# Optimization experiments

Measured on AMD Instinct MI355X. Metric: run time of the kernel, lower is better.

The kernel has to match this reference:

```python
import jax, jax.numpy as jnp
import numpy as np

D_MODEL = 1024
NUM_HEADS = 16
D_K = D_MODEL // NUM_HEADS
ROPE_THETA = 10000.0


def setup_inputs() -> dict:
    key = jax.random.key(0)
    kx, kq, kk, kv, ko = jax.random.split(key, 5)
    B, S = 4, 2048
    std = (2.0 / (D_MODEL + D_MODEL)) ** 0.5
    def w(k):
        return jax.random.truncated_normal(k, -3.0, 3.0, (D_MODEL, D_MODEL), jnp.float32) * std
    return {
        "x": jax.random.normal(kx, (B, S, D_MODEL), jnp.float32),
        "Wq": w(kq), "Wk": w(kk), "Wv": w(kv), "Wo": w(ko),
    }


def _apply_rope(t):
    # t: [B, H, S, d_k]
    S, dk = t.shape[-2], t.shape[-1]
    inv_freq = 1.0 / (ROPE_THETA ** (jnp.arange(0, dk, 2) / dk))  # [dk/2]
    angles = jnp.outer(jnp.arange(S), inv_freq)                    # [S, dk/2]
    cos = jnp.repeat(jnp.cos(angles), 2, axis=-1).astype(t.dtype)  # [S, dk]
    sin = jnp.repeat(jnp.sin(angles), 2, axis=-1).astype(t.dtype)
    t_even = t[..., 0::2]
    t_odd = t[..., 1::2]
    t_rot = jnp.stack([-t_odd, t_even], axis=-1).reshape(t.shape)
    return t * cos + t_rot * sin


def reference(x, Wq, Wk, Wv, Wo):
    B, S, D = x.shape
    H, dk = NUM_HEADS, D_K
    q = jnp.einsum("bsi,io->bso", x, Wq).reshape(B, S, H, dk).swapaxes(1, 2)
    k = jnp.einsum("bsi,io->bso", x, Wk).reshape(B, S, H, dk).swapaxes(1, 2)
    v = jnp.einsum("bsi,io->bso", x, Wv).reshape(B, S, H, dk).swapaxes(1, 2)
    q = _apply_rope(q)
    k = _apply_rope(k)
    scores = jnp.einsum("bhqd,bhkd->bhqk", q, k) / (dk ** 0.5)  # [B,H,S,S]
    causal = jnp.tril(jnp.ones((S, S), dtype=bool))
    scores = jnp.where(causal, scores, -jnp.inf)
    attn = jax.nn.softmax(scores, axis=-1)
    out = jnp.einsum("bhqk,bhkd->bhqd", attn, v)  # [B,H,S,dk]
    out = out.swapaxes(1, 2).reshape(B, S, D)
    return jnp.einsum("bsi,io->bso", out, Wo)
```

## Files before the change

kernel.cpp:

```cpp
#include <hip/hip_runtime.h>
#include <hip/hip_bf16.h>

#define SEQ   2048
#define NB    4
#define NH    16
#define DK    64
#define DM    1024
#define MROWS (NB * SEQ)

typedef __bf16 bf16_t;
typedef __bf16 bf16x8 __attribute__((ext_vector_type(8)));
typedef __bf16 bf16x4 __attribute__((ext_vector_type(4)));
typedef float  f32x4  __attribute__((ext_vector_type(4)));

#define MFMA16(a, b, c) __builtin_amdgcn_mfma_f32_16x16x32_bf16((a), (b), (c), 0, 0, 0)

__device__ __forceinline__ void gl2lds16(const bf16_t* g, bf16_t* l) {
    __builtin_amdgcn_global_load_lds(
        (const __attribute__((address_space(1))) unsigned int*)g,
        (__attribute__((address_space(3))) unsigned int*)l, 16, 0, 0);
}

#define SBAR()   asm volatile("s_barrier" ::: "memory")
#define VMC(N)   asm volatile("s_waitcnt vmcnt(" #N ")" ::: "memory")

__global__ __launch_bounds__(256) void cvt_kernel(
    const float* __restrict__ in, bf16_t* __restrict__ out, int n)
{
    int i = (blockIdx.x * 256 + threadIdx.x) * 4;
    if (i + 3 < n) {
        const float4 v = *(const float4*)(in + i);
        bf16x4 o;
        o[0] = (bf16_t)v.x; o[1] = (bf16_t)v.y;
        o[2] = (bf16_t)v.z; o[3] = (bf16_t)v.w;
        *(bf16x4*)(out + i) = o;
    }
}

__global__ __launch_bounds__(256) void wtr_kernel(
    const float* __restrict__ W, bf16_t* __restrict__ Wt)
{
    __shared__ float T[32][33];
    const int tk0 = (blockIdx.x >> 5) << 5;
    const int tn0 = (blockIdx.x & 31) << 5;
    const int r = threadIdx.x >> 5, c = threadIdx.x & 31;
#pragma unroll
    for (int i = 0; i < 4; ++i)
        T[r + i * 8][c] = W[(size_t)(tk0 + r + i * 8) * DM + tn0 + c];
    __syncthreads();
#pragma unroll
    for (int i = 0; i < 4; ++i)
        Wt[(size_t)(tn0 + r + i * 8) * DM + tk0 + c] = (bf16_t)T[c][r + i * 8];
}

__global__ void rope_table_kernel(float2* __restrict__ tab) {
    int idx = blockIdx.x * 256 + threadIdx.x;
    if (idx >= SEQ * 32) return;
    int s = idx >> 5, i = idx & 31;
    float freq = powf(10000.0f, -(float)i / 32.0f);
    float a = (float)s * freq;
    tab[idx] = make_float2(cosf(a), sinf(a));
}

template<bool TR>
__device__ __forceinline__ void kloop(
    const bf16_t* __restrict__ Xp, const bf16_t* __restrict__ Wp,
    bf16_t* L, int tid, f32x4 (&acc)[8][4])
{
    const int lane = tid & 63;
    const int wave = tid >> 6;
    const int wm   = wave >> 2;
    const int wn   = wave & 3;
    const int lrow = lane & 15;
    const int lcol = (lane >> 4) << 3;

    bf16_t* const AR = L;
    bf16_t* const BR = L + 32768;

    const bf16_t* pA0 = Xp + (size_t)(wave * 16 + lrow) * DM + lcol;
    const bf16_t* pA1 = pA0 + (size_t)128 * DM;
    const bf16_t* pB0 = Wp + (size_t)(wave * 16 + lrow) * DM + lcol;
    const bf16_t* pB1 = pB0 + (size_t)128 * DM;

    bf16_t* const adst = AR + wave * 1024;
    bf16_t* const bdst = BR + wave * 1024;

    const bf16_t* const Ard = AR + wm * 8192;
    const bf16_t* const Brd = BR + wn * 4096;

    bf16x8 a0[2][2], a1[2][2], bc[4][2], bn[4][2];

#define RD_A(BUF, Q, D)                                                       \
    D[0][0] = *(const bf16x8*)(Ard + (BUF) + (2*(Q)+0)*1024 + lane*8);        \
    D[0][1] = *(const bf16x8*)(Ard + (BUF) + (2*(Q)+0)*1024 + 512 + lane*8);  \
    D[1][0] = *(const bf16x8*)(Ard + (BUF) + (2*(Q)+1)*1024 + lane*8);        \
    D[1][1] = *(const bf16x8*)(Ard + (BUF) + (2*(Q)+1)*1024 + 512 + lane*8);

#define RD_B(BUF, NF, D)                                                      \
    D[NF][0] = *(const bf16x8*)(Brd + (BUF) + (NF)*1024 + lane*8);            \
    D[NF][1] = *(const bf16x8*)(Brd + (BUF) + (NF)*1024 + 512 + lane*8);

#define ST_A(BUF, H, C)                                                       \
    gl2lds16(((H) ? pA1 : pA0) + (C),      adst + (BUF) + (H)*8192);          \
    gl2lds16(((H) ? pA1 : pA0) + (C) + 32, adst + (BUF) + (H)*8192 + 512);

#define ST_B(BUF, H, C)                                                       \
    gl2lds16(((H) ? pB1 : pB0) + (C),      bdst + (BUF) + (H)*8192);          \
    gl2lds16(((H) ? pB1 : pB0) + (C) + 32, bdst + (BUF) + (H)*8192 + 512);

#define QMMA(Q, A, B)                                                         \
    __builtin_amdgcn_s_setprio(1);                                            \
    _Pragma("unroll")                                                         \
    for (int nf = 0; nf < 4; ++nf) {                                          \
        if (TR) {                                                             \
            acc[2*(Q)][nf]   = MFMA16(B[nf][0], A[0][0], acc[2*(Q)][nf]);     \
            acc[2*(Q)][nf]   = MFMA16(B[nf][1], A[0][1], acc[2*(Q)][nf]);     \
            acc[2*(Q)+1][nf] = MFMA16(B[nf][0], A[1][0], acc[2*(Q)+1][nf]);   \
            acc[2*(Q)+1][nf] = MFMA16(B[nf][1], A[1][1], acc[2*(Q)+1][nf]);   \
        } else {                                                              \
            acc[2*(Q)][nf]   = MFMA16(A[0][0], B[nf][0], acc[2*(Q)][nf]);     \
            acc[2*(Q)][nf]   = MFMA16(A[0][1], B[nf][1], acc[2*(Q)][nf]);     \
            acc[2*(Q)+1][nf] = MFMA16(A[1][0], B[nf][0], acc[2*(Q)+1][nf]);   \
            acc[2*(Q)+1][nf] = MFMA16(A[1][1], B[nf][1], acc[2*(Q)+1][nf]);   \
        }                                                                     \
    }                                                                         \
    __builtin_amdgcn_s_setprio(0);

#define ITER(LST)                                                             \
                                                              \
    VMC(4); SBAR();                                                           \
    RD_A(0, 1, a1) RD_B(16384, 0, bn)                                         \
    if (!(LST)) { ST_B(0, 0, 128) }                                           \
    QMMA(0, a0, bc)                                                           \
                                                              \
    SBAR();                                                                   \
    RD_A(0, 2, a0) RD_B(16384, 1, bn)                                         \
    if (!(LST)) { ST_B(0, 1, 128) }                                           \
    QMMA(1, a1, bc)                                                           \
                                                              \
    SBAR();                                                                   \
    RD_A(0, 3, a1) RD_B(16384, 2, bn)                                         \
    QMMA(2, a0, bc)                                                           \
                                                              \
    if (LST) { VMC(0); } else { VMC(4); }                                     \
    SBAR();                                                                   \
    RD_A(16384, 0, a0) RD_B(16384, 3, bn)                                     \
    if (!(LST)) { ST_A(0, 0, 128) }                                           \
    QMMA(3, a1, bc)                                                           \
                                                            \
    if (!(LST)) { VMC(2); }                                                   \
    SBAR();                                                                   \
    RD_A(16384, 1, a1) RD_B(0, 0, bc)                                         \
    if (!(LST)) { ST_A(0, 1, 128) }                                           \
    QMMA(0, a0, bn)                                                           \
                                                            \
    SBAR();                                                                   \
    RD_A(16384, 2, a0) RD_B(0, 1, bc)                                         \
    if (!(LST)) { ST_B(16384, 0, 192) }                                       \
    QMMA(1, a1, bn)                                                           \
                                                            \
    SBAR();                                                                   \
    RD_A(16384, 3, a1) RD_B(0, 2, bc)                                         \
    if (!(LST)) { ST_B(16384, 1, 192) }                                       \
    QMMA(2, a0, bn)                                                           \
                                                            \
    if (!(LST)) { VMC(4); }                                                   \
    SBAR();                                                                   \
    RD_A(0, 0, a0) RD_B(0, 3, bc)                                             \
    if (!(LST)) { ST_A(16384, 0, 192) ST_A(16384, 1, 192) }                   \
    QMMA(3, a1, bn)

    ST_A(0, 0, 0) ST_A(0, 1, 0)
    ST_B(0, 0, 0) ST_B(0, 1, 0)
    ST_B(16384, 0, 64) ST_B(16384, 1, 64)
    ST_A(16384, 0, 64) ST_A(16384, 1, 64)
    VMC(8);
    SBAR();
    RD_A(0, 0, a0)
    RD_B(0, 0, bc) RD_B(0, 1, bc) RD_B(0, 2, bc) RD_B(0, 3, bc)

    for (int it = 0; it < 7; ++it) {
        ITER(0)
        pA0 += 128; pA1 += 128; pB0 += 128; pB1 += 128;
    }
    ITER(1)

#undef ITER
#undef QMMA
#undef ST_B
#undef ST_A
#undef RD_B
#undef RD_A
}

__global__ __launch_bounds__(512, 2) void gemm_qkv_kernel(
    const bf16_t* __restrict__ X, const bf16_t* __restrict__ Wt,
    bf16_t* __restrict__ Qt, bf16_t* __restrict__ Kt, bf16_t* __restrict__ Vtr,
    const float2* __restrict__ rope)
{
    __shared__ __align__(16) bf16_t L[65536];

    const int tid = threadIdx.x;
    const int xcd = blockIdx.x & 7;
    const int idx = blockIdx.x >> 3;
    const int mt  = xcd * 4 + (idx & 3);
    const int nt  = idx >> 2;
    const int m0 = mt << 8, n0 = nt << 8;
    const bool tr = (n0 >= 2 * DM);

    f32x4 acc[8][4] = {};
    if (tr) kloop<true >(X + (size_t)m0 * DM, Wt + (size_t)n0 * DM, L, tid, acc);
    else    kloop<false>(X + (size_t)m0 * DM, Wt + (size_t)n0 * DM, L, tid, acc);

    const int lane = tid & 63;
    const int wave = tid >> 6;
    const int wm   = wave >> 2, wn = wave & 3;
    const int l    = lane & 15;
    const int quad = lane >> 4;

#pragma unroll
    for (int mf = 0; mf < 8; ++mf)
#pragma unroll
        for (int nf = 0; nf < 4; ++nf)
#pragma unroll
            for (int r = 0; r < 4; ++r) {
                float v = acc[mf][nf][r];
                if (tr) {
                    const int n = n0 + wn * 64 + nf * 16 + quad * 4 + r;
                    const int m = m0 + wm * 128 + mf * 16 + l;
                    const int bi = m >> 11, s = m & (SEQ - 1);
                    const int col = n & (DM - 1);
                    const int h = col >> 6, d = col & (DK - 1);
                    Vtr[(((size_t)(bi * NH + h)) * DK + d) * SEQ + s] = (bf16_t)v;
                } else {
                    const int m  = m0 + wm * 128 + mf * 16 + quad * 4 + r;
                    const int nn = n0 + wn * 64 + nf * 16 + l;
                    const int bi = m >> 11, s = m & (SEQ - 1);
                    const int col = nn & (DM - 1);
                    const int h = col >> 6, d = col & (DK - 1);
                    float pv = __shfl_xor(v, 1);
                    float2 cs = rope[s * 32 + (d >> 1)];
                    float res = (d & 1) ? (v * cs.x + pv * cs.y)
                                        : (v * cs.x - pv * cs.y);
                    bf16_t* dst = (nn < DM) ? Qt : Kt;
                    if (nn < DM) res *= 0.125f;
                    dst[(((size_t)(bi * NH + h)) * SEQ + s) * DK + d] = (bf16_t)res;
                }
            }
}

__global__ __launch_bounds__(512, 2) void gemm_out_kernel(
    const bf16_t* __restrict__ X, const bf16_t* __restrict__ Wt,
    float* __restrict__ out)
{
    __shared__ __align__(16) bf16_t L[65536];

    const int tid = threadIdx.x;
    const int xcd = blockIdx.x & 7;
    const int idx = blockIdx.x >> 3;
    const int mt  = xcd * 4 + (idx & 3);
    const int nt  = idx >> 2;
    const int m0 = mt << 8, n0 = nt << 8;

    f32x4 acc[8][4] = {};
    kloop<false>(X + (size_t)m0 * DM, Wt + (size_t)n0 * DM, L, tid, acc);

    const int lane = tid & 63;
    const int wave = tid >> 6;
    const int wm   = wave >> 2, wn = wave & 3;
    const int l    = lane & 15;
    const int quad = lane >> 4;

#pragma unroll
    for (int mf = 0; mf < 8; ++mf)
#pragma unroll
        for (int nf = 0; nf < 4; ++nf)
#pragma unroll
            for (int r = 0; r < 4; ++r) {
                const int m  = m0 + wm * 128 + mf * 16 + quad * 4 + r;
                const int nn = n0 + wn * 64 + nf * 16 + l;
                out[(size_t)m * DM + nn] = acc[mf][nf][r];
            }
}

#define KLD 72

__global__ __launch_bounds__(256) void attn_kernel(
    const bf16_t* __restrict__ Q, const bf16_t* __restrict__ K,
    const bf16_t* __restrict__ Vt, bf16_t* __restrict__ O)
{
    __shared__ __align__(16) bf16_t Kl[64 * KLD];
    __shared__ __align__(16) bf16_t Vl[64 * KLD];
    __shared__ __align__(16) bf16_t Pl[4][32 * KLD];

    const int bh   = blockIdx.x;
    const int qx   = blockIdx.y;
    const int tid  = threadIdx.x;
    const int wave = tid >> 6;
    const int lane = tid & 63;
    const int l    = lane & 15;
    const int quad = lane >> 4;
    const int srow = tid >> 3;
    const int sch  = (tid & 7) << 3;

    bf16_t* Pw = Pl[wave];
    const bf16_t* Qb = Q  + (size_t)bh * SEQ * DK;
    const bf16_t* Kb = K  + (size_t)bh * SEQ * DK;
    const bf16_t* Vb = Vt + (size_t)bh * DK * SEQ;
    const int b = bh >> 4, h = bh & 15;

    for (int ph = 0; ph < 2; ++ph) {
        const int qblk = ph ? (15 - qx) : qx;
        const int q0w  = qblk * 128 + wave * 32;
        const int nch  = 2 * (qblk + 1);

        bf16x8 qb[2][2];
#pragma unroll
        for (int u = 0; u < 2; ++u) {
            qb[u][0] = *(const bf16x8*)(Qb + (size_t)(q0w + u * 16 + l) * DK + quad * 8);
            qb[u][1] = *(const bf16x8*)(Qb + (size_t)(q0w + u * 16 + l) * DK + 32 + quad * 8);
        }

        float m_run[2] = {-3e38f, -3e38f};
        float l_run[2] = {0.f, 0.f};
        f32x4 o[4][2] = {};

        bf16x8 pk0 = *(const bf16x8*)(Kb + (size_t)srow * DK + sch);
        bf16x8 pk1 = *(const bf16x8*)(Kb + (size_t)(32 + srow) * DK + sch);
        bf16x8 pv0 = *(const bf16x8*)(Vb + (size_t)srow * SEQ + sch);
        bf16x8 pv1 = *(const bf16x8*)(Vb + (size_t)(32 + srow) * SEQ + sch);

        for (int i = 0; i < nch; ++i) {
            const int c = i * 64;
            __syncthreads();
            *(bf16x8*)(Kl + srow * KLD + sch)        = pk0;
            *(bf16x8*)(Kl + (32 + srow) * KLD + sch) = pk1;
            *(bf16x8*)(Vl + srow * KLD + sch)        = pv0;
            *(bf16x8*)(Vl + (32 + srow) * KLD + sch) = pv1;
            __syncthreads();
            if (i + 1 < nch) {
                const int cn = c + 64;
                pk0 = *(const bf16x8*)(Kb + (size_t)(cn + srow) * DK + sch);
                pk1 = *(const bf16x8*)(Kb + (size_t)(cn + 32 + srow) * DK + sch);
                pv0 = *(const bf16x8*)(Vb + (size_t)srow * SEQ + cn + sch);
                pv1 = *(const bf16x8*)(Vb + (size_t)(32 + srow) * SEQ + cn + sch);
            }
            if (c > q0w + 31) continue;

            f32x4 st[4][2] = {};
#pragma unroll
            for (int t = 0; t < 4; ++t) {
                const bf16x8 k0 = *(const bf16x8*)(Kl + (t * 16 + l) * KLD + quad * 8);
                const bf16x8 k1 = *(const bf16x8*)(Kl + (t * 16 + l) * KLD + 32 + quad * 8);
                st[t][0] = MFMA16(k0, qb[0][0], st[t][0]);
                st[t][0] = MFMA16(k1, qb[0][1], st[t][0]);
                st[t][1] = MFMA16(k0, qb[1][0], st[t][1]);
                st[t][1] = MFMA16(k1, qb[1][1], st[t][1]);
            }
            if (c + 63 > q0w) {
#pragma unroll
                for (int u = 0; u < 2; ++u) {
                    const int thr = q0w + u * 16 + l - c - quad * 4;
#pragma unroll
                    for (int t = 0; t < 4; ++t)
#pragma unroll
                        for (int r = 0; r < 4; ++r)
                            if (t * 16 + r > thr) st[t][u][r] = -3e38f;
                }
            }
#pragma unroll
            for (int u = 0; u < 2; ++u) {
                float cmax = -3e38f;
#pragma unroll
                for (int t = 0; t < 4; ++t)
#pragma unroll
                    for (int r = 0; r < 4; ++r)
                        cmax = fmaxf(cmax, st[t][u][r]);
                cmax = fmaxf(cmax, __shfl_xor(cmax, 16));
                cmax = fmaxf(cmax, __shfl_xor(cmax, 32));
                const float mnew  = fmaxf(m_run[u], cmax);
                const float alpha = __expf(m_run[u] - mnew);
                m_run[u] = mnew;
                float csum = 0.f;
#pragma unroll
                for (int t = 0; t < 4; ++t)
#pragma unroll
                    for (int r = 0; r < 4; ++r) {
                        st[t][u][r] = __expf(st[t][u][r] - mnew);
                        csum += st[t][u][r];
                    }
                csum += __shfl_xor(csum, 16);
                csum += __shfl_xor(csum, 32);
                l_run[u] = l_run[u] * alpha + csum;
#pragma unroll
                for (int n = 0; n < 4; ++n)
#pragma unroll
                    for (int r = 0; r < 4; ++r)
                        o[n][u][r] *= alpha;
#pragma unroll
                for (int t = 0; t < 4; ++t) {
                    bf16x4 pk;
                    pk[0] = (bf16_t)st[t][u][0]; pk[1] = (bf16_t)st[t][u][1];
                    pk[2] = (bf16_t)st[t][u][2]; pk[3] = (bf16_t)st[t][u][3];
                    *(bf16x4*)(Pw + (u * 16 + l) * KLD + t * 16 + quad * 4) = pk;
                }
            }
            const bf16x8 pb00 = *(const bf16x8*)(Pw + l * KLD + quad * 8);
            const bf16x8 pb01 = *(const bf16x8*)(Pw + l * KLD + 32 + quad * 8);
            const bf16x8 pb10 = *(const bf16x8*)(Pw + (16 + l) * KLD + quad * 8);
            const bf16x8 pb11 = *(const bf16x8*)(Pw + (16 + l) * KLD + 32 + quad * 8);
#pragma unroll
            for (int n = 0; n < 4; ++n) {
                const bf16x8 v0 = *(const bf16x8*)(Vl + (n * 16 + l) * KLD + quad * 8);
                const bf16x8 v1 = *(const bf16x8*)(Vl + (n * 16 + l) * KLD + 32 + quad * 8);
                o[n][0] = MFMA16(v0, pb00, o[n][0]);
                o[n][0] = MFMA16(v1, pb01, o[n][0]);
                o[n][1] = MFMA16(v0, pb10, o[n][1]);
                o[n][1] = MFMA16(v1, pb11, o[n][1]);
            }
        }

#pragma unroll
        for (int u = 0; u < 2; ++u) {
            const float inv = 1.0f / l_run[u];
#pragma unroll
            for (int n = 0; n < 4; ++n) {
                bf16x4 ov;
                ov[0] = (bf16_t)(o[n][u][0] * inv); ov[1] = (bf16_t)(o[n][u][1] * inv);
                ov[2] = (bf16_t)(o[n][u][2] * inv); ov[3] = (bf16_t)(o[n][u][3] * inv);
                *(bf16x4*)(Pw + (u * 16 + l) * KLD + n * 16 + quad * 4) = ov;
            }
        }
        const int row  = lane >> 1;
        const int half = (lane & 1) * 32;
        const bf16x8 w0 = *(const bf16x8*)(Pw + row * KLD + half);
        const bf16x8 w1 = *(const bf16x8*)(Pw + row * KLD + half + 8);
        const bf16x8 w2 = *(const bf16x8*)(Pw + row * KLD + half + 16);
        const bf16x8 w3 = *(const bf16x8*)(Pw + row * KLD + half + 24);
        bf16_t* op = O + ((size_t)(b * SEQ + qblk * 128 + wave * 32 + row)) * DM
                       + h * DK + half;
        *(bf16x8*)(op)      = w0;
        *(bf16x8*)(op + 8)  = w1;
        *(bf16x8*)(op + 16) = w2;
        *(bf16x8*)(op + 24) = w3;
    }
}

extern "C" void kernel_launch(void* const* d_in, const int* in_sizes, int n_in,
                              void* d_out, int out_size, void* d_ws, size_t ws_size,
                              hipStream_t stream)
{
    const float* x  = (const float*)d_in[0];
    const float* Wq = (const float*)d_in[1];
    const float* Wk = (const float*)d_in[2];
    const float* Wv = (const float*)d_in[3];
    const float* Wo = (const float*)d_in[4];

    char* ws = (char*)d_ws;
    float2* rope = (float2*)ws;
    const size_t TEN = (size_t)MROWS * DM;
    const size_t WEL = (size_t)DM * DM;
    bf16_t* xb    = (bf16_t*)(ws + (1 << 19));
    bf16_t* Wqkvt = xb + TEN;
    bf16_t* Wot   = Wqkvt + 3 * WEL;
    bf16_t* Qt    = Wot + WEL;
    bf16_t* Kt    = Qt + TEN;
    bf16_t* Vt    = Kt + TEN;
    bf16_t* Ot    = Vt + TEN;

    rope_table_kernel<<<(SEQ * 32 + 255) / 256, 256, 0, stream>>>(rope);

    cvt_kernel<<<(int)(TEN / 4 / 256), 256, 0, stream>>>(x, xb, (int)TEN);
    wtr_kernel<<<1024, 256, 0, stream>>>(Wq, Wqkvt);
    wtr_kernel<<<1024, 256, 0, stream>>>(Wk, Wqkvt + WEL);
    wtr_kernel<<<1024, 256, 0, stream>>>(Wv, Wqkvt + 2 * WEL);
    wtr_kernel<<<1024, 256, 0, stream>>>(Wo, Wot);

    gemm_qkv_kernel<<<32 * 12, 512, 0, stream>>>(xb, Wqkvt, Qt, Kt, Vt, rope);

    attn_kernel<<<dim3(NB * NH, 8), 256, 0, stream>>>(Qt, Kt, Vt, Ot);

    gemm_out_kernel<<<32 * 4, 512, 0, stream>>>(Ot, Wot, (float*)d_out);
}
```

Before: 313.1 us.

## Restructure GEMM main loop into barrier-fenced phases without register double-buffering

Replaces the register double-buffered (a0/a1, bc/bn) software pipeline in the GEMM mainloop with a single set of fragment registers. Each phase now reads LDS fragments, issues the next global-to-LDS loads, waits on lgkmcnt, and runs the MFMAs behind barriers and sched_barrier fences. The loop becomes a plain 8-iteration loop instead of a peeled last iteration, and the load order of the prologue changes. This lowers register pressure and gives a more predictable schedule, but adds many extra barriers and stops LDS reads from overlapping MFMA work within a wave.

```diff
diff --git a/kernel.cpp b/kernel.cpp
--- a/kernel.cpp
+++ b/kernel.cpp
@@ -21,8 +21,11 @@
         (__attribute__((address_space(3))) unsigned int*)l, 16, 0, 0);
 }
 
-#define SBAR()   asm volatile("s_barrier" ::: "memory")
-#define VMC(N)   asm volatile("s_waitcnt vmcnt(" #N ")" ::: "memory")
+#define BAR()   __builtin_amdgcn_s_barrier()
+#define SCB()   __builtin_amdgcn_sched_barrier(0)
+#define LGK0()  asm volatile("s_waitcnt lgkmcnt(0)")
+#define LGK8()  asm volatile("s_waitcnt lgkmcnt(8)")
+#define VMC(N)  asm volatile("s_waitcnt vmcnt(" #N ")")
 
 __global__ __launch_bounds__(256) void cvt_kernel(
     const float* __restrict__ in, bf16_t* __restrict__ out, int n)
@@ -88,17 +91,17 @@
     const bf16_t* const Ard = AR + wm * 8192;
     const bf16_t* const Brd = BR + wn * 4096;
 
-    bf16x8 a0[2][2], a1[2][2], bc[4][2], bn[4][2];
-
-#define RD_A(BUF, Q, D)                                                       \
-    D[0][0] = *(const bf16x8*)(Ard + (BUF) + (2*(Q)+0)*1024 + lane*8);        \
-    D[0][1] = *(const bf16x8*)(Ard + (BUF) + (2*(Q)+0)*1024 + 512 + lane*8);  \
-    D[1][0] = *(const bf16x8*)(Ard + (BUF) + (2*(Q)+1)*1024 + lane*8);        \
-    D[1][1] = *(const bf16x8*)(Ard + (BUF) + (2*(Q)+1)*1024 + 512 + lane*8);
-
-#define RD_B(BUF, NF, D)                                                      \
-    D[NF][0] = *(const bf16x8*)(Brd + (BUF) + (NF)*1024 + lane*8);            \
-    D[NF][1] = *(const bf16x8*)(Brd + (BUF) + (NF)*1024 + 512 + lane*8);
+    bf16x8 a[2][2], bc[4][2];
+
+#define RD_A(BUF, Q)                                                          \
+    a[0][0] = *(const bf16x8*)(Ard + (BUF) + (2*(Q)+0)*1024 + lane*8);        \
+    a[0][1] = *(const bf16x8*)(Ard + (BUF) + (2*(Q)+0)*1024 + 512 + lane*8);  \
+    a[1][0] = *(const bf16x8*)(Ard + (BUF) + (2*(Q)+1)*1024 + lane*8);        \
+    a[1][1] = *(const bf16x8*)(Ard + (BUF) + (2*(Q)+1)*1024 + 512 + lane*8);
+
+#define RD_B(BUF, NF)                                                         \
+    bc[NF][0] = *(const bf16x8*)(Brd + (BUF) + (NF)*1024 + lane*8);           \
+    bc[NF][1] = *(const bf16x8*)(Brd + (BUF) + (NF)*1024 + 512 + lane*8);
 
 #define ST_A(BUF, H, C)                                                       \
     gl2lds16(((H) ? pA1 : pA0) + (C),      adst + (BUF) + (H)*8192);          \
@@ -108,84 +111,87 @@
     gl2lds16(((H) ? pB1 : pB0) + (C),      bdst + (BUF) + (H)*8192);          \
     gl2lds16(((H) ? pB1 : pB0) + (C) + 32, bdst + (BUF) + (H)*8192 + 512);
 
-#define QMMA(Q, A, B)                                                         \
+#define QMMA(Q)                                                               \
     __builtin_amdgcn_s_setprio(1);                                            \
     _Pragma("unroll")                                                         \
     for (int nf = 0; nf < 4; ++nf) {                                          \
         if (TR) {                                                             \
-            acc[2*(Q)][nf]   = MFMA16(B[nf][0], A[0][0], acc[2*(Q)][nf]);     \
-            acc[2*(Q)][nf]   = MFMA16(B[nf][1], A[0][1], acc[2*(Q)][nf]);     \
-            acc[2*(Q)+1][nf] = MFMA16(B[nf][0], A[1][0], acc[2*(Q)+1][nf]);   \
-            acc[2*(Q)+1][nf] = MFMA16(B[nf][1], A[1][1], acc[2*(Q)+1][nf]);   \
+            acc[2*(Q)][nf]   = MFMA16(bc[nf][0], a[0][0], acc[2*(Q)][nf]);    \
+            acc[2*(Q)][nf]   = MFMA16(bc[nf][1], a[0][1], acc[2*(Q)][nf]);    \
+            acc[2*(Q)+1][nf] = MFMA16(bc[nf][0], a[1][0], acc[2*(Q)+1][nf]);  \
+            acc[2*(Q)+1][nf] = MFMA16(bc[nf][1], a[1][1], acc[2*(Q)+1][nf]);  \
         } else {                                                              \
-            acc[2*(Q)][nf]   = MFMA16(A[0][0], B[nf][0], acc[2*(Q)][nf]);     \
-            acc[2*(Q)][nf]   = MFMA16(A[0][1], B[nf][1], acc[2*(Q)][nf]);     \
-            acc[2*(Q)+1][nf] = MFMA16(A[1][0], B[nf][0], acc[2*(Q)+1][nf]);   \
-            acc[2*(Q)+1][nf] = MFMA16(A[1][1], B[nf][1], acc[2*(Q)+1][nf]);   \
+            acc[2*(Q)][nf]   = MFMA16(a[0][0], bc[nf][0], acc[2*(Q)][nf]);    \
+            acc[2*(Q)][nf]   = MFMA16(a[0][1], bc[nf][1], acc[2*(Q)][nf]);    \
+            acc[2*(Q)+1][nf] = MFMA16(a[1][0], bc[nf][0], acc[2*(Q)+1][nf]);  \
+            acc[2*(Q)+1][nf] = MFMA16(a[1][1], bc[nf][1], acc[2*(Q)+1][nf]);  \
         }                                                                     \
     }                                                                         \
     __builtin_amdgcn_s_setprio(0);
 
-#define ITER(LST)                                                             \
-                                                              \
-    VMC(4); SBAR();                                                           \
-    RD_A(0, 1, a1) RD_B(16384, 0, bn)                                         \
-    if (!(LST)) { ST_B(0, 0, 128) }                                           \
-    QMMA(0, a0, bc)                                                           \
-                                                              \
-    SBAR();                                                                   \
-    RD_A(0, 2, a0) RD_B(16384, 1, bn)                                         \
-    if (!(LST)) { ST_B(0, 1, 128) }                                           \
-    QMMA(1, a1, bc)                                                           \
-                                                              \
-    SBAR();                                                                   \
-    RD_A(0, 3, a1) RD_B(16384, 2, bn)                                         \
-    QMMA(2, a0, bc)                                                           \
-                                                              \
-    if (LST) { VMC(0); } else { VMC(4); }                                     \
-    SBAR();                                                                   \
-    RD_A(16384, 0, a0) RD_B(16384, 3, bn)                                     \
-    if (!(LST)) { ST_A(0, 0, 128) }                                           \
-    QMMA(3, a1, bc)                                                           \
-                                                            \
-    if (!(LST)) { VMC(2); }                                                   \
-    SBAR();                                                                   \
-    RD_A(16384, 1, a1) RD_B(0, 0, bc)                                         \
-    if (!(LST)) { ST_A(0, 1, 128) }                                           \
-    QMMA(0, a0, bn)                                                           \
-                                                            \
-    SBAR();                                                                   \
-    RD_A(16384, 2, a0) RD_B(0, 1, bc)                                         \
-    if (!(LST)) { ST_B(16384, 0, 192) }                                       \
-    QMMA(1, a1, bn)                                                           \
-                                                            \
-    SBAR();                                                                   \
-    RD_A(16384, 3, a1) RD_B(0, 2, bc)                                         \
-    if (!(LST)) { ST_B(16384, 1, 192) }                                       \
-    QMMA(2, a0, bn)                                                           \
-                                                            \
-    if (!(LST)) { VMC(4); }                                                   \
-    SBAR();                                                                   \
-    RD_A(0, 0, a0) RD_B(0, 3, bc)                                             \
-    if (!(LST)) { ST_A(16384, 0, 192) ST_A(16384, 1, 192) }                   \
-    QMMA(3, a1, bn)
-
-    ST_A(0, 0, 0) ST_A(0, 1, 0)
-    ST_B(0, 0, 0) ST_B(0, 1, 0)
+    ST_B(0, 0, 0)      ST_B(0, 1, 0)
+    ST_A(0, 0, 0)      ST_A(0, 1, 0)
     ST_B(16384, 0, 64) ST_B(16384, 1, 64)
-    ST_A(16384, 0, 64) ST_A(16384, 1, 64)
-    VMC(8);
-    SBAR();
-    RD_A(0, 0, a0)
-    RD_B(0, 0, bc) RD_B(0, 1, bc) RD_B(0, 2, bc) RD_B(0, 3, bc)
-
-    for (int it = 0; it < 7; ++it) {
-        ITER(0)
+    VMC(4);
+    BAR();
+
+    for (int it = 0; it < 8; ++it) {
+        const bool lst = (it == 7);
+
+        RD_A(0, 0) RD_B(0, 0) RD_B(0, 1) RD_B(0, 2) RD_B(0, 3)
+        ST_A(16384, 0, 64) ST_A(16384, 1, 64)
+        LGK8();
+        BAR(); LGK0(); SCB();
+        QMMA(0)
+        BAR();
+
+        RD_A(0, 1)
+        if (!lst) { ST_B(0, 0, 128) }
+        BAR(); LGK0(); SCB();
+        QMMA(1)
+        BAR();
+
+        RD_A(0, 2)
+        if (!lst) { ST_B(0, 1, 128) }
+        BAR(); LGK0(); SCB();
+        QMMA(2)
+        BAR();
+
+        RD_A(0, 3)
+        BAR(); LGK0(); SCB();
+        QMMA(3)
+        if (lst) { VMC(0); } else { VMC(4); }
+        BAR();
+
+        RD_A(16384, 0) RD_B(16384, 0) RD_B(16384, 1) RD_B(16384, 2) RD_B(16384, 3)
+        if (!lst) { ST_A(0, 0, 128) }
+        LGK8();
+        BAR(); LGK0(); SCB();
+        QMMA(0)
+        BAR();
+
+        RD_A(16384, 1)
+        if (!lst) { ST_A(0, 1, 128) }
+        BAR(); LGK0(); SCB();
+        QMMA(1)
+        BAR();
+
+        RD_A(16384, 2)
+        if (!lst) { ST_B(16384, 0, 192) }
+        BAR(); LGK0(); SCB();
+        QMMA(2)
+        BAR();
+
+        RD_A(16384, 3)
+        if (!lst) { ST_B(16384, 1, 192) }
+        BAR(); LGK0(); SCB();
+        QMMA(3)
+        if (!lst) { VMC(4); }
+        BAR();
+
         pA0 += 128; pA1 += 128; pB0 += 128; pB1 += 128;
     }
-    ITER(1)
-
-#undef ITER
+
 #undef QMMA
 #undef ST_B
 #undef ST_A
```

Result: no change. 310.3 us (-0.9%).
